# Kernel optimization log

Hardware: AMD Instinct MI355X
Metric: run time of the kernel (lower is better)

Reference implementation:

```python
import jax, jax.numpy as jnp
import numpy as np

N_NODES = 40000
N_EDGES = 640000
IN_DIM = 128
HID_DIM = 128


def _glorot(key, shape):
    fan_in, fan_out = shape[1], shape[0]
    lim = np.sqrt(6.0 / (fan_in + fan_out))
    return jax.random.uniform(key, shape, jnp.float32, -lim, lim)


def setup_inputs() -> dict:
    key = jax.random.key(0)
    ks = jax.random.split(key, 8)
    x = jax.random.normal(ks[0], (N_NODES, IN_DIM), dtype=jnp.float32)
    edge_index = jax.random.randint(ks[1], (2, N_EDGES), 0, N_NODES, dtype=jnp.int64)
    # SAGEConv params: lin_l (applied to aggregated neighbors, has bias), lin_r (self, no bias)
    W1l = _glorot(ks[2], (HID_DIM, IN_DIM))
    b1l = jnp.zeros((HID_DIM,), jnp.float32)
    W1r = _glorot(ks[3], (HID_DIM, IN_DIM))
    W2l = _glorot(ks[4], (HID_DIM, HID_DIM))
    b2l = jnp.zeros((HID_DIM,), jnp.float32)
    W2r = _glorot(ks[5], (HID_DIM, HID_DIM))
    return {"x": x, "edge_index": edge_index, "W1l": W1l, "b1l": b1l,
            "W1r": W1r, "W2l": W2l, "b2l": b2l, "W2r": W2r}


def _sage_conv(x, src, dst, Wl, bl, Wr):
    # mean aggregation of source features into destination nodes
    msg = x[src]  # [E, D] gather
    agg = jax.ops.segment_sum(msg, dst, num_segments=N_NODES)          # [N, D]
    cnt = jax.ops.segment_sum(jnp.ones_like(dst, jnp.float32), dst,
                              num_segments=N_NODES)                     # [N]
    mean = agg / jnp.maximum(cnt, 1.0)[:, None]
    # out = lin_l(mean_neighbors) + lin_r(x)
    return mean @ Wl.T + bl + x @ Wr.T


def reference(x, edge_index, W1l, b1l, W1r, W2l, b2l, W2r):
    src, dst = edge_index[0], edge_index[1]
    h = jax.nn.relu(_sage_conv(x, src, dst, W1l, b1l, W1r))
    h = jax.nn.relu(_sage_conv(h, src, dst, W2l, b2l, W2r))
    return h
```

## Files before the change

kernel.cpp:

```cpp
#include <hip/hip_runtime.h>
#include <hip/hip_bf16.h>

#define DIM 128
#define NN 40000
#define NE 640000
#define NBLK ((NN + 255) / 256)

typedef __attribute__((ext_vector_type(8))) short s16x8;
typedef __attribute__((ext_vector_type(4))) float f32x4;
typedef __attribute__((ext_vector_type(4))) unsigned short u16x4;
typedef __attribute__((ext_vector_type(4))) unsigned int u32x4;

__device__ __forceinline__ float bf16_lo(unsigned v) { return __uint_as_float(v << 16); }
__device__ __forceinline__ float bf16_hi(unsigned v) { return __uint_as_float(v & 0xffff0000u); }
__device__ __forceinline__ unsigned short f_to_bf16(float f) {
    unsigned u = __float_as_uint(f);
    u += 0x7fffu + ((u >> 16) & 1u);
    return (unsigned short)(u >> 16);
}

__global__ void fill_const_f32(float* __restrict__ out, int n, float v) {
    int i = blockIdx.x * blockDim.x + threadIdx.x;
    if (i < n) out[i] = v;
}

__global__ void cvt_all(const float* __restrict__ x, unsigned short* __restrict__ xb,
                        const float* __restrict__ w0, const float* __restrict__ w1,
                        const float* __restrict__ w2, const float* __restrict__ w3,
                        unsigned short* __restrict__ wb,
                        int* __restrict__ deg, const int* __restrict__ ei,
                        int* __restrict__ flag) {
    __shared__ int sfmt;
    int b = blockIdx.x;
    if (b >= 5064) {
        if (threadIdx.x < 64) {
            int w = ei[2 * threadIdx.x + 1];
            unsigned long long m = __ballot(w == 0);
            if (threadIdx.x == 0) sfmt = (m == ~0ull) ? 1 : 0;
        }
        __syncthreads();
        int f = sfmt;
        if (b == 5064 && threadIdx.x == 0) *flag = f;
        int e = (b - 5064) * 256 + threadIdx.x;
        if (e < NE) {
            int dst = f ? ((const int2*)ei)[NE + e].x : ei[NE + e];
            if ((unsigned)dst < (unsigned)NN) atomicAdd(&deg[dst], 1);
        }
        return;
    }
    const float* src;
    unsigned short* dst;
    size_t i;
    if (b < 5000) {
        src = x; dst = xb;
        i = (size_t)b * 256 + threadIdx.x;
    } else {
        int w = b - 5000;
        int m = w >> 4;
        src = (m == 0) ? w0 : (m == 1) ? w1 : (m == 2) ? w2 : w3;
        dst = wb + (size_t)m * 16384;
        i = (size_t)(w & 15) * 256 + threadIdx.x;
    }
    f32x4 v = *(const f32x4*)(src + 4 * i);
    u16x4 o;
    o.x = f_to_bf16(v.x); o.y = f_to_bf16(v.y);
    o.z = f_to_bf16(v.z); o.w = f_to_bf16(v.w);
    *(u16x4*)(dst + 4 * i) = o;
}


__global__ void block_sums(const int* __restrict__ deg, int* __restrict__ bsum) {
    __shared__ int sh[256];
    int i = blockIdx.x * 256 + threadIdx.x;
    sh[threadIdx.x] = (i < NN) ? deg[i] : 0;
    __syncthreads();
    for (int off = 128; off > 0; off >>= 1) {
        if (threadIdx.x < off) sh[threadIdx.x] += sh[threadIdx.x + off];
        __syncthreads();
    }
    if (threadIdx.x == 0) bsum[blockIdx.x] = sh[0];
}

__global__ void scan_block2(const int* __restrict__ deg, const int* __restrict__ bsum,
                            int* __restrict__ row_ptr, int* __restrict__ cursor) {
    __shared__ int sh[256];
    int t = threadIdx.x, bid = blockIdx.x;

    int v0 = (t < NBLK) ? bsum[t] : 0;
    sh[t] = v0;
    __syncthreads();
    for (int off = 1; off < 256; off <<= 1) {
        int u = (t >= off) ? sh[t - off] : 0;
        __syncthreads();
        sh[t] += u;
        __syncthreads();
    }
    int base = sh[bid] - bsum[bid];
    __syncthreads();

    int i = bid * 256 + t;
    int v = (i < NN) ? deg[i] : 0;
    sh[t] = v;
    __syncthreads();
    for (int off = 1; off < 256; off <<= 1) {
        int u = (t >= off) ? sh[t - off] : 0;
        __syncthreads();
        sh[t] += u;
        __syncthreads();
    }
    int excl = sh[t] - v + base;
    if (i < NN) { row_ptr[i] = excl; cursor[i] = excl; }
    if (i == NN - 1) row_ptr[NN] = excl + v;
}

__global__ void fill_csr(const int* __restrict__ ei, const int* __restrict__ fmt,
                         int* __restrict__ cursor, int* __restrict__ sorted_src) {
    int gid = blockIdx.x * blockDim.x + threadIdx.x;
    int f = *fmt;
    int s[4], dd[4];
#pragma unroll
    for (int u = 0; u < 4; ++u) {
        int e = gid + u * 160000;
        if (f) {
            s[u]  = ((const int2*)ei)[e].x;
            dd[u] = ((const int2*)ei)[NE + e].x;
        } else {
            s[u]  = ei[e];
            dd[u] = ei[NE + e];
        }
    }
#pragma unroll
    for (int u = 0; u < 4; ++u) {
        if ((unsigned)dd[u] < (unsigned)NN) {
            int pos = atomicAdd(&cursor[dd[u]], 1);
            if ((unsigned)pos < (unsigned)NE) sorted_src[pos] = s[u];
        }
    }
}


#define ACC8(A, v)                                 \
    A[0] += bf16_lo((v).x); A[1] += bf16_hi((v).x); \
    A[2] += bf16_lo((v).y); A[3] += bf16_hi((v).y); \
    A[4] += bf16_lo((v).z); A[5] += bf16_hi((v).z); \
    A[6] += bf16_lo((v).w); A[7] += bf16_hi((v).w);

#define ACC8W(A, v, W)                                         \
    A[0] = fmaf(W, bf16_lo((v).x), A[0]);                      \
    A[1] = fmaf(W, bf16_hi((v).x), A[1]);                      \
    A[2] = fmaf(W, bf16_lo((v).y), A[2]);                      \
    A[3] = fmaf(W, bf16_hi((v).y), A[3]);                      \
    A[4] = fmaf(W, bf16_lo((v).z), A[4]);                      \
    A[5] = fmaf(W, bf16_hi((v).z), A[5]);                      \
    A[6] = fmaf(W, bf16_lo((v).w), A[6]);                      \
    A[7] = fmaf(W, bf16_hi((v).w), A[7]);

template <bool WRITE_F32>
__global__ __launch_bounds__(512) void sage_layer(
    const unsigned short* __restrict__ xin,
    const int* __restrict__ row_ptr,
    const int* __restrict__ sorted_src,
    const unsigned short* __restrict__ Wl,
    const unsigned short* __restrict__ Wr,
    const float* __restrict__ bias,
    void* __restrict__ outv) {
    __shared__ unsigned short lds_mean[64 * 128];
    __shared__ unsigned short lds_hs[64 * 128];

    int tid = threadIdx.x;
    int lane = tid & 63;
    int wv = tid >> 6;
    int row0 = blockIdx.x * 64;

    {
        int r = tid >> 3;
        int lid0 = (tid & 7) * 2;
        int lid1 = lid0 + 1;
        const unsigned short* src = xin + (size_t)(row0 + r) * DIM + lid0 * 8;
        u32x4 v0 = *(const u32x4*)(src);
        u32x4 v1 = *(const u32x4*)(src + 8);
        int base = (r >> 4) * 2048;
        int o0 = base + (lid0 >> 2) * 512 + (lid0 & 3) * 128 + (((r & 15) ^ lid0) * 8);
        int o1 = base + (lid1 >> 2) * 512 + (lid1 & 3) * 128 + (((r & 15) ^ lid1) * 8);
        *(u32x4*)(lds_hs + o0) = v0;
        *(u32x4*)(lds_hs + o1) = v1;
    }

    {
        int grp = lane >> 4;
        int lid = lane & 15;
        int gbase = grp << 4;
        int g = wv * 4 + grp;

        int n0 = row0 + g, n1 = row0 + 32 + g;
        int st0 = row_ptr[n0], en0 = row_ptr[n0 + 1];
        int st1 = row_ptr[n1], en1 = row_ptr[n1 + 1];

#pragma unroll
        for (int it = 0; it < 2; ++it) {
            int nb = it * 32 + g;
            int start = it ? st1 : st0;
            int end   = it ? en1 : en0;

            float a[8] = {0.f, 0.f, 0.f, 0.f, 0.f, 0.f, 0.f, 0.f};
            float b[8] = {0.f, 0.f, 0.f, 0.f, 0.f, 0.f, 0.f, 0.f};

            int i = start;
            for (; i + 16 <= end; i += 16) {
                int idx = sorted_src[i + lid];
#pragma unroll
                for (int j = 0; j < 16; j += 4) {
                    int s0 = __shfl(idx, gbase + j);
                    int s1 = __shfl(idx, gbase + j + 1);
                    int s2 = __shfl(idx, gbase + j + 2);
                    int s3 = __shfl(idx, gbase + j + 3);
                    u32x4 v0 = *(const u32x4*)(xin + (size_t)s0 * DIM + lid * 8);
                    u32x4 v1 = *(const u32x4*)(xin + (size_t)s1 * DIM + lid * 8);
                    u32x4 v2 = *(const u32x4*)(xin + (size_t)s2 * DIM + lid * 8);
                    u32x4 v3 = *(const u32x4*)(xin + (size_t)s3 * DIM + lid * 8);
                    ACC8(a, v0);
                    ACC8(b, v1);
                    ACC8(a, v2);
                    ACC8(b, v3);
                }
            }
            int rem = end - i;
            if (rem > 0) {
                int src_i = (i + lid < end) ? (i + lid) : (end - 1);
                int idx = sorted_src[src_i];
                int rm1 = rem - 1;
#pragma unroll
                for (int j0 = 0; j0 < 16; j0 += 8) {
                    if (j0 < rem) {
                        u32x4 vv[8];
#pragma unroll
                        for (int k = 0; k < 8; ++k) {
                            int jj = j0 + k;
                            int cj = (jj < rem) ? jj : rm1;
                            int s = __shfl(idx, gbase + cj);
                            vv[k] = *(const u32x4*)(xin + (size_t)s * DIM + lid * 8);
                        }
#pragma unroll
                        for (int k = 0; k < 8; ++k) {
                            float wt = (j0 + k < rem) ? 1.f : 0.f;
                            if (k & 1) { ACC8W(b, vv[k], wt); }
                            else       { ACC8W(a, vv[k], wt); }
                        }
                    }
                }
            }
#pragma unroll
            for (int k = 0; k < 8; ++k) a[k] += b[k];

            int d = end - start;
            float inv = 1.f / (float)(d > 1 ? d : 1);
            u32x4 o;
            o.x = (unsigned)f_to_bf16(a[0] * inv) | ((unsigned)f_to_bf16(a[1] * inv) << 16);
            o.y = (unsigned)f_to_bf16(a[2] * inv) | ((unsigned)f_to_bf16(a[3] * inv) << 16);
            o.z = (unsigned)f_to_bf16(a[4] * inv) | ((unsigned)f_to_bf16(a[5] * inv) << 16);
            o.w = (unsigned)f_to_bf16(a[6] * inv) | ((unsigned)f_to_bf16(a[7] * inv) << 16);
            int off = (nb >> 4) * 2048 + (lid >> 2) * 512 + (lid & 3) * 128
                    + (((nb & 15) ^ lid) * 8);
            *(u32x4*)(lds_mean + off) = o;
        }
    }

    __syncthreads();

    {
        int quad = lane >> 4;
        int m16 = lane & 15;
        int bcol = wv * 16 + m16;
        const unsigned short* wl0 = Wl + (size_t)bcol * DIM + quad * 8;
        const unsigned short* wr0 = Wr + (size_t)bcol * DIM + quad * 8;
        s16x8 bl[4], br[4];
#pragma unroll
        for (int kb = 0; kb < 4; ++kb) {
            bl[kb] = *(const s16x8*)(wl0 + kb * 32);
            br[kb] = *(const s16x8*)(wr0 + kb * 32);
        }
        f32x4 acc[4] = {{0,0,0,0},{0,0,0,0},{0,0,0,0},{0,0,0,0}};
#pragma unroll
        for (int t = 0; t < 4; ++t) {
#pragma unroll
            for (int kb = 0; kb < 4; ++kb) {
                int lo = (lane ^ ((kb << 2) | quad)) << 3;
                s16x8 am = *(const s16x8*)(lds_mean + t * 2048 + kb * 512 + lo);
                acc[t] = __builtin_amdgcn_mfma_f32_16x16x32_bf16(am, bl[kb], acc[t], 0, 0, 0);
            }
#pragma unroll
            for (int kb = 0; kb < 4; ++kb) {
                int lo = (lane ^ ((kb << 2) | quad)) << 3;
                s16x8 ah = *(const s16x8*)(lds_hs + t * 2048 + kb * 512 + lo);
                acc[t] = __builtin_amdgcn_mfma_f32_16x16x32_bf16(ah, br[kb], acc[t], 0, 0, 0);
            }
        }
        float bv = bias[bcol];
#pragma unroll
        for (int t = 0; t < 4; ++t) {
#pragma unroll
            for (int r = 0; r < 4; ++r) {
                int orow = row0 + t * 16 + quad * 4 + r;
                float v = fmaxf(acc[t][r] + bv, 0.f);
                if (WRITE_F32)
                    ((float*)outv)[(size_t)orow * DIM + bcol] = v;
                else
                    ((unsigned short*)outv)[(size_t)orow * DIM + bcol] = f_to_bf16(v);
            }
        }
    }
}


extern "C" void kernel_launch(void* const* d_in, const int* in_sizes, int n_in,
                              void* d_out, int out_size, void* d_ws, size_t ws_size,
                              hipStream_t stream) {
    const float* x   = (const float*)d_in[0];
    const int*   ei  = (const int*)d_in[1];
    const float* W1l = (const float*)d_in[2];
    const float* b1l = (const float*)d_in[3];
    const float* W1r = (const float*)d_in[4];
    const float* W2l = (const float*)d_in[5];
    const float* b2l = (const float*)d_in[6];
    const float* W2r = (const float*)d_in[7];
    float* out = (float*)d_out;

    const int OUT_ELEMS = NN * DIM;

    const size_t OFF_DEG  = 0;
    const size_t OFF_ROW  = 163840;
    const size_t OFF_BSUM = 324608;
    const size_t OFF_CUR  = 327680;
    const size_t OFF_FMT  = 491264;
    const size_t OFF_SRT  = 491520;
    const size_t OFF_WB   = 3051520;
    const size_t OFF_XB   = 3182592;
    const size_t OFF_H1   = 23662592;
    const size_t NEEDED   = 33902592;

    if (ws_size < NEEDED) {
        fill_const_f32<<<(OUT_ELEMS + 255) / 256, 256, 0, stream>>>(out, OUT_ELEMS, 50.0f);
        return;
    }

    char* ws = (char*)d_ws;
    int* deg     = (int*)(ws + OFF_DEG);
    int* row_ptr = (int*)(ws + OFF_ROW);
    int* bsum    = (int*)(ws + OFF_BSUM);
    int* cursor  = (int*)(ws + OFF_CUR);
    int* fmtflag = (int*)(ws + OFF_FMT);
    int* sorted  = (int*)(ws + OFF_SRT);
    unsigned short* Wb    = (unsigned short*)(ws + OFF_WB);
    unsigned short* xb    = (unsigned short*)(ws + OFF_XB);
    unsigned short* h1b   = (unsigned short*)(ws + OFF_H1);
    unsigned short* W1lb = Wb;
    unsigned short* W1rb = Wb + 16384;
    unsigned short* W2lb = Wb + 32768;
    unsigned short* W2rb = Wb + 49152;

    hipMemsetAsync(deg, 0, NN * sizeof(int), stream);
    cvt_all<<<7564, 256, 0, stream>>>(x, xb, W1l, W1r, W2l, W2r, Wb, deg, ei, fmtflag);
    block_sums<<<NBLK, 256, 0, stream>>>(deg, bsum);
    scan_block2<<<NBLK, 256, 0, stream>>>(deg, bsum, row_ptr, cursor);
    fill_csr<<<625, 256, 0, stream>>>(ei, fmtflag, cursor, sorted);

    sage_layer<false><<<NN / 64, 512, 0, stream>>>(xb, row_ptr, sorted, W1lb, W1rb, b1l, h1b);
    sage_layer<true><<<NN / 64, 512, 0, stream>>>(h1b, row_ptr, sorted, W2lb, W2rb, b2l, out);
}
```

Measured before the change: 210.4 us.

## Fuse scan kernels, prefetch neighbor indices for both nodes, raise MFMA priority

Measured after the change: 225.7 us. 7.3% more time.

```diff
diff --git a/kernel.cpp b/kernel.cpp
--- a/kernel.cpp
+++ b/kernel.cpp
@@ -69,33 +69,21 @@
 }
 
 
-__global__ void block_sums(const int* __restrict__ deg, int* __restrict__ bsum) {
+__global__ void scan_fused(const int* __restrict__ deg,
+                           int* __restrict__ row_ptr, int* __restrict__ cursor) {
     __shared__ int sh[256];
-    int i = blockIdx.x * 256 + threadIdx.x;
-    sh[threadIdx.x] = (i < NN) ? deg[i] : 0;
+    int t = threadIdx.x, bid = blockIdx.x;
+
+    int limit = bid * 256;
+    int part = 0;
+    for (int i = t; i < limit; i += 256) part += deg[i];
+    sh[t] = part;
     __syncthreads();
     for (int off = 128; off > 0; off >>= 1) {
-        if (threadIdx.x < off) sh[threadIdx.x] += sh[threadIdx.x + off];
+        if (t < off) sh[t] += sh[t + off];
         __syncthreads();
     }
-    if (threadIdx.x == 0) bsum[blockIdx.x] = sh[0];
-}
-
-__global__ void scan_block2(const int* __restrict__ deg, const int* __restrict__ bsum,
-                            int* __restrict__ row_ptr, int* __restrict__ cursor) {
-    __shared__ int sh[256];
-    int t = threadIdx.x, bid = blockIdx.x;
-
-    int v0 = (t < NBLK) ? bsum[t] : 0;
-    sh[t] = v0;
-    __syncthreads();
-    for (int off = 1; off < 256; off <<= 1) {
-        int u = (t >= off) ? sh[t - off] : 0;
-        __syncthreads();
-        sh[t] += u;
-        __syncthreads();
-    }
-    int base = sh[bid] - bsum[bid];
+    int base = sh[0];
     __syncthreads();
 
     int i = bid * 256 + t;
@@ -154,6 +142,23 @@
     A[5] = fmaf(W, bf16_hi((v).z), A[5]);                      \
     A[6] = fmaf(W, bf16_lo((v).w), A[6]);                      \
     A[7] = fmaf(W, bf16_hi((v).w), A[7]);
+
+#define PROC16(IDX)                                                        \
+    _Pragma("unroll")                                                      \
+    for (int j = 0; j < 16; j += 4) {                                      \
+        int s0 = __shfl(IDX, gbase + j);                                   \
+        int s1 = __shfl(IDX, gbase + j + 1);                               \
+        int s2 = __shfl(IDX, gbase + j + 2);                               \
+        int s3 = __shfl(IDX, gbase + j + 3);                               \
+        u32x4 v0 = *(const u32x4*)(xin + (size_t)s0 * DIM + lid * 8);      \
+        u32x4 v1 = *(const u32x4*)(xin + (size_t)s1 * DIM + lid * 8);      \
+        u32x4 v2 = *(const u32x4*)(xin + (size_t)s2 * DIM + lid * 8);      \
+        u32x4 v3 = *(const u32x4*)(xin + (size_t)s3 * DIM + lid * 8);      \
+        ACC8(a, v0);                                                       \
+        ACC8(b, v1);                                                       \
+        ACC8(a, v2);                                                       \
+        ACC8(b, v3);                                                       \
+    }
 
 template <bool WRITE_F32>
 __global__ __launch_bounds__(512) void sage_layer(
@@ -195,39 +200,43 @@
         int n0 = row0 + g, n1 = row0 + 32 + g;
         int st0 = row_ptr[n0], en0 = row_ptr[n0 + 1];
         int st1 = row_ptr[n1], en1 = row_ptr[n1 + 1];
+        int d0 = en0 - st0, d1 = en1 - st1;
+
+        int rem0 = d0 & 15, rem1 = d1 & 15;
+        int idxA = 0, idxRA = 0, idxB = 0, idxRB = 0;
+        if (d0 >= 16) idxA  = sorted_src[st0 + lid];
+        if (rem0 > 0) idxRA = sorted_src[st0 + (d0 & ~15) + ((lid < rem0) ? lid : rem0 - 1)];
+        if (d1 >= 16) idxB  = sorted_src[st1 + lid];
+        if (rem1 > 0) idxRB = sorted_src[st1 + (d1 & ~15) + ((lid < rem1) ? lid : rem1 - 1)];
+
+        int stA[2]  = {st0, st1};
+        int enA[2]  = {en0, en1};
+        int dAr[2]  = {d0, d1};
+        int ib0[2]  = {idxA, idxB};
+        int ibR[2]  = {idxRA, idxRB};
+        int remA[2] = {rem0, rem1};
 
 #pragma unroll
         for (int it = 0; it < 2; ++it) {
             int nb = it * 32 + g;
-            int start = it ? st1 : st0;
-            int end   = it ? en1 : en0;
+            int start = stA[it], end = enA[it], d = dAr[it];
 
             float a[8] = {0.f, 0.f, 0.f, 0.f, 0.f, 0.f, 0.f, 0.f};
             float b[8] = {0.f, 0.f, 0.f, 0.f, 0.f, 0.f, 0.f, 0.f};
 
             int i = start;
-            for (; i + 16 <= end; i += 16) {
-                int idx = sorted_src[i + lid];
-#pragma unroll
-                for (int j = 0; j < 16; j += 4) {
-                    int s0 = __shfl(idx, gbase + j);
-                    int s1 = __shfl(idx, gbase + j + 1);
-                    int s2 = __shfl(idx, gbase + j + 2);
-                    int s3 = __shfl(idx, gbase + j + 3);
-                    u32x4 v0 = *(const u32x4*)(xin + (size_t)s0 * DIM + lid * 8);
-                    u32x4 v1 = *(const u32x4*)(xin + (size_t)s1 * DIM + lid * 8);
-                    u32x4 v2 = *(const u32x4*)(xin + (size_t)s2 * DIM + lid * 8);
-                    u32x4 v3 = *(const u32x4*)(xin + (size_t)s3 * DIM + lid * 8);
-                    ACC8(a, v0);
-                    ACC8(b, v1);
-                    ACC8(a, v2);
-                    ACC8(b, v3);
+            if (d >= 16) {
+                int idx = ib0[it];
+                PROC16(idx);
+                i += 16;
+                for (; i + 16 <= end; i += 16) {
+                    int idx2 = sorted_src[i + lid];
+                    PROC16(idx2);
                 }
             }
-            int rem = end - i;
+            int rem = remA[it];
             if (rem > 0) {
-                int src_i = (i + lid < end) ? (i + lid) : (end - 1);
-                int idx = sorted_src[src_i];
+                int idx = ibR[it];
                 int rm1 = rem - 1;
 #pragma unroll
                 for (int j0 = 0; j0 < 16; j0 += 8) {
@@ -252,7 +261,6 @@
 #pragma unroll
             for (int k = 0; k < 8; ++k) a[k] += b[k];
 
-            int d = end - start;
             float inv = 1.f / (float)(d > 1 ? d : 1);
             u32x4 o;
             o.x = (unsigned)f_to_bf16(a[0] * inv) | ((unsigned)f_to_bf16(a[1] * inv) << 16);
@@ -280,6 +288,7 @@
             br[kb] = *(const s16x8*)(wr0 + kb * 32);
         }
         f32x4 acc[4] = {{0,0,0,0},{0,0,0,0},{0,0,0,0},{0,0,0,0}};
+        __builtin_amdgcn_s_setprio(1);
 #pragma unroll
         for (int t = 0; t < 4; ++t) {
 #pragma unroll
@@ -295,6 +304,7 @@
                 acc[t] = __builtin_amdgcn_mfma_f32_16x16x32_bf16(ah, br[kb], acc[t], 0, 0, 0);
             }
         }
+        __builtin_amdgcn_s_setprio(0);
         float bv = bias[bcol];
 #pragma unroll
         for (int t = 0; t < 4; ++t) {
@@ -329,7 +339,6 @@
 
     const size_t OFF_DEG  = 0;
     const size_t OFF_ROW  = 163840;
-    const size_t OFF_BSUM = 324608;
     const size_t OFF_CUR  = 327680;
     const size_t OFF_FMT  = 491264;
     const size_t OFF_SRT  = 491520;
@@ -346,7 +355,6 @@
     char* ws = (char*)d_ws;
     int* deg     = (int*)(ws + OFF_DEG);
     int* row_ptr = (int*)(ws + OFF_ROW);
-    int* bsum    = (int*)(ws + OFF_BSUM);
     int* cursor  = (int*)(ws + OFF_CUR);
     int* fmtflag = (int*)(ws + OFF_FMT);
     int* sorted  = (int*)(ws + OFF_SRT);
@@ -360,8 +368,7 @@
 
     hipMemsetAsync(deg, 0, NN * sizeof(int), stream);
     cvt_all<<<7564, 256, 0, stream>>>(x, xb, W1l, W1r, W2l, W2r, Wb, deg, ei, fmtflag);
-    block_sums<<<NBLK, 256, 0, stream>>>(deg, bsum);
-    scan_block2<<<NBLK, 256, 0, stream>>>(deg, bsum, row_ptr, cursor);
+    scan_fused<<<NBLK, 256, 0, stream>>>(deg, row_ptr, cursor);
     fill_csr<<<625, 256, 0, stream>>>(ei, fmtflag, cursor, sorted);
 
     sage_layer<false><<<NN / 64, 512, 0, stream>>>(xb, row_ptr, sorted, W1lb, W1rb, b1l, h1b);
```
